# Performance work log

Measured on AMD Instinct MI355X. Metric: run time of the kernel, lower is better.

## Reference

```python
import jax, jax.numpy as jnp
import numpy as np

COMMITMENT_COST = 0.25
NUM_EMBEDDINGS = 512
EMBEDDING_DIM = 64


def setup_inputs() -> dict:
    key = jax.random.key(0)
    k1, k2 = jax.random.split(key)
    inputs = jax.random.normal(k1, (64, EMBEDDING_DIM, 32, 32), dtype=jnp.float32)
    # nn.Embedding init: uniform(-1/K, 1/K)
    emb_w = jax.random.uniform(
        k2, (NUM_EMBEDDINGS, EMBEDDING_DIM), dtype=jnp.float32,
        minval=-1.0 / NUM_EMBEDDINGS, maxval=1.0 / NUM_EMBEDDINGS)
    return {"inputs": inputs, "emb_w": emb_w}


def reference(inputs, emb_w):
    sg = jax.lax.stop_gradient
    # NCHW -> NHWC
    x = jnp.transpose(inputs, (0, 2, 3, 1))          # [B, H, W, D]
    B, H, W, D = x.shape
    flat = x.reshape(-1, D)                          # [N, D]
    dist = (jnp.sum(flat * flat, axis=1, keepdims=True)
            + jnp.sum(emb_w * emb_w, axis=1)
            - 2.0 * jnp.dot(flat, emb_w.T))          # [N, K]
    idx = jnp.argmin(dist, axis=1)                   # [N]
    # one-hot @ emb_w is just a gather
    quantized = emb_w[idx].reshape(B, H, W, D)       # [B, H, W, D]
    e_latent_loss = jnp.mean((sg(quantized) - x) ** 2)
    q_latent_loss = jnp.mean((quantized - sg(x)) ** 2)
    loss = q_latent_loss + COMMITMENT_COST * e_latent_loss
    # straight-through estimator
    quantized_st = x + sg(quantized - x)
    out = jnp.transpose(quantized_st, (0, 3, 1, 2))  # back to NCHW
    return loss, out, idx[:, None]
```

## Files before the change

### kernel.cpp

```cpp
#include <hip/hip_runtime.h>


#define D_    64
#define HW_   1024
#define N_    65536
#define K_    512
#define M_    128
#define CH_   128
#define NCH_  4
#define NDTOT (N_ * D_)

__global__ __launch_bounds__(256) void vq_norm_kernel(const float* __restrict__ emb,
                                                      float* __restrict__ wsn) {
    int k = blockIdx.x * 256 + threadIdx.x;
    if (k < K_) {
        const float* e = emb + k * D_;
        float r[8];
#pragma unroll
        for (int j = 0; j < 8; ++j) r[j] = __fmul_rn(e[j], e[j]);
#pragma unroll
        for (int i = 1; i < 8; ++i)
#pragma unroll
            for (int j = 0; j < 8; ++j)
                r[j] = __fadd_rn(r[j], __fmul_rn(e[i * 8 + j], e[i * 8 + j]));
        float s = __fadd_rn(__fadd_rn(__fadd_rn(r[0], r[1]), __fadd_rn(r[2], r[3])),
                            __fadd_rn(__fadd_rn(r[4], r[5]), __fadd_rn(r[6], r[7])));
        wsn[k] = s;
    }
}

__global__ __launch_bounds__(256, 2) void vq_main_kernel(const float* __restrict__ inp,
                                                         const float* __restrict__ emb,
                                                         const float* __restrict__ wsn,
                                                         float* __restrict__ out) {
    __shared__ float lds[16520];
    float* ldsx = lds;
    float* ldse = lds + 8192;
    float* sxs  = lds + 16384;
    float* partial = lds + 16512;

    const int tid = threadIdx.x;
    const int pg  = tid & 15;
    const int kg  = tid >> 4;
    const int n0  = blockIdx.x * M_;
    const int b   = n0 >> 10;
    const int hw0 = n0 & 1023;
    const float* xbase = inp + b * (D_ * HW_) + hw0;

#pragma unroll
    for (int i = 0; i < 8; ++i) {
        int q  = i * 256 + tid;
        int d  = q >> 5;
        int pq = q & 31;
        float4 v = *(const float4*)(xbase + d * HW_ + pq * 4);
        *(float4*)(ldsx + d * M_ + pq * 4) = v;
    }
    __syncthreads();

    if (tid < M_) {
        float r[8];
#pragma unroll
        for (int j = 0; j < 8; ++j) {
            float v = ldsx[j * M_ + tid];
            r[j] = __fmul_rn(v, v);
        }
#pragma unroll
        for (int i = 1; i < 8; ++i)
#pragma unroll
            for (int j = 0; j < 8; ++j) {
                float v = ldsx[(i * 8 + j) * M_ + tid];
                r[j] = __fadd_rn(r[j], __fmul_rn(v, v));
            }
        sxs[tid] = __fadd_rn(__fadd_rn(__fadd_rn(r[0], r[1]), __fadd_rn(r[2], r[3])),
                             __fadd_rn(__fadd_rn(r[4], r[5]), __fadd_rn(r[6], r[7])));
    }
    __syncthreads();

    float sxp[8];
#pragma unroll
    for (int pp = 0; pp < 8; ++pp) sxp[pp] = sxs[pg * 8 + pp];

    float runv[8];
    int   runi[8];
#pragma unroll
    for (int pp = 0; pp < 8; ++pp) { runv[pp] = 3.4e38f; runi[pp] = 0; }

    for (int c = 0; c < NCH_; ++c) {
        __syncthreads();
#pragma unroll
        for (int i = 0; i < 8; ++i) {
            int q  = i * 256 + tid;
            int kl = q & 127;
            int dq = q >> 7;
            float4 v = *(const float4*)(emb + (c * CH_ + kl) * D_ + dq * 4);
            ldse[(dq * 4 + 0) * CH_ + kl] = v.x;
            ldse[(dq * 4 + 1) * CH_ + kl] = v.y;
            ldse[(dq * 4 + 2) * CH_ + kl] = v.z;
            ldse[(dq * 4 + 3) * CH_ + kl] = v.w;
        }
        float4 nh0 = *(const float4*)(wsn + c * CH_ + kg * 8);
        float4 nh1 = *(const float4*)(wsn + c * CH_ + kg * 8 + 4);
        __syncthreads();

        float acc[8][8];
#pragma unroll
        for (int pp = 0; pp < 8; ++pp)
#pragma unroll
            for (int kk = 0; kk < 8; ++kk) acc[pp][kk] = 0.f;

#pragma unroll 2
        for (int d = 0; d < D_; ++d) {
            float4 xa = *(const float4*)(ldsx + d * M_ + pg * 8);
            float4 xb = *(const float4*)(ldsx + d * M_ + pg * 8 + 4);
            float4 ea = *(const float4*)(ldse + d * CH_ + kg * 8);
            float4 eb = *(const float4*)(ldse + d * CH_ + kg * 8 + 4);
            float xr[8] = {xa.x, xa.y, xa.z, xa.w, xb.x, xb.y, xb.z, xb.w};
            float er[8] = {ea.x, ea.y, ea.z, ea.w, eb.x, eb.y, eb.z, eb.w};
#pragma unroll
            for (int pp = 0; pp < 8; ++pp)
#pragma unroll
                for (int kk = 0; kk < 8; ++kk)
                    acc[pp][kk] = fmaf(xr[pp], er[kk], acc[pp][kk]);
        }

        float nk[8] = {nh0.x, nh0.y, nh0.z, nh0.w, nh1.x, nh1.y, nh1.z, nh1.w};
#pragma unroll
        for (int pp = 0; pp < 8; ++pp) {
            float sx = sxp[pp];
#pragma unroll
            for (int kk = 0; kk < 8; ++kk) {
                float t1 = __fadd_rn(sx, nk[kk]);
                float v  = __fadd_rn(t1, -2.0f * acc[pp][kk]);
                if (v < runv[pp]) { runv[pp] = v; runi[pp] = c * CH_ + kg * 8 + kk; }
            }
        }
    }

    __syncthreads();
    float* sv = ldse;
    int*   si = (int*)(ldse + 2048);
    int*   fi = (int*)(ldse + 4096);
#pragma unroll
    for (int pp = 0; pp < 8; ++pp) {
        sv[kg * M_ + pg * 8 + pp] = runv[pp];
        si[kg * M_ + pg * 8 + pp] = runi[pp];
    }
    __syncthreads();
    if (tid < M_) {
        float bv = 3.4e38f; int bi = 0x7fffffff;
#pragma unroll
        for (int g = 0; g < 16; ++g) {
            float v  = sv[g * M_ + tid];
            int   ii = si[g * M_ + tid];
            if (v < bv || (v == bv && ii < bi)) { bv = v; bi = ii; }
        }
        fi[tid] = bi;
        out[1 + NDTOT + n0 + tid] = (float)bi;
    }
    __syncthreads();

    float* obase = out + 1 + b * (D_ * HW_) + hw0;
    float local = 0.f;
    for (int i = 0; i < 32; ++i) {
        int q = i * 256 + tid;
        int d = q >> 7;
        int p = q & 127;
        int idx = fi[p];
        float e  = emb[idx * D_ + d];
        float xv = ldsx[d * M_ + p];
        float df = e - xv;
        local = fmaf(df, df, local);
        obase[d * HW_ + p] = e;
    }
#pragma unroll
    for (int off = 32; off > 0; off >>= 1)
        local += __shfl_down(local, off, 64);
    if ((tid & 63) == 0) partial[tid >> 6] = local;
    __syncthreads();
    if (tid == 0) {
        float t = partial[0] + partial[1] + partial[2] + partial[3];
        atomicAdd(out, t * (1.25f / (float)NDTOT));
    }
}

extern "C" void kernel_launch(void* const* d_in, const int* in_sizes, int n_in,
                              void* d_out, int out_size, void* d_ws, size_t ws_size,
                              hipStream_t stream) {
    const float* inp = (const float*)d_in[0];
    const float* emb = (const float*)d_in[1];
    float* out = (float*)d_out;
    float* wsn = (float*)d_ws;

    hipMemsetAsync(d_out, 0, sizeof(float), stream);
    vq_norm_kernel<<<2, 256, 0, stream>>>(emb, wsn);
    vq_main_kernel<<<512, 256, 0, stream>>>(inp, emb, wsn, out);
}
```

Measured before the change: 132.1 us.

## Fuse codebook-norm kernel into main VQ kernel and vectorize gather epilogue

Drops the separate norm kernel and has every block compute all 512 codebook norms into LDS, which removes one launch and the workspace round-trip at the cost of redundant per-block norm work. The thread-to-tile mapping is changed so each wave covers an 8x8 patch of points and codes. The reduction scratch gets a padded stride to avoid LDS bank conflicts. The final gather now reads each code row as float4 with a fixed point per thread instead of scalar loads. NDTOT is redefined to an equal value.

```diff
diff --git a/kernel.cpp b/kernel.cpp
--- a/kernel.cpp
+++ b/kernel.cpp
@@ -8,40 +8,26 @@
 #define M_    128
 #define CH_   128
 #define NCH_  4
-#define NDTOT (N_ * D_)
-
-__global__ __launch_bounds__(256) void vq_norm_kernel(const float* __restrict__ emb,
-                                                      float* __restrict__ wsn) {
-    int k = blockIdx.x * 256 + threadIdx.x;
-    if (k < K_) {
-        const float* e = emb + k * D_;
-        float r[8];
-#pragma unroll
-        for (int j = 0; j < 8; ++j) r[j] = __fmul_rn(e[j], e[j]);
-#pragma unroll
-        for (int i = 1; i < 8; ++i)
-#pragma unroll
-            for (int j = 0; j < 8; ++j)
-                r[j] = __fadd_rn(r[j], __fmul_rn(e[i * 8 + j], e[i * 8 + j]));
-        float s = __fadd_rn(__fadd_rn(__fadd_rn(r[0], r[1]), __fadd_rn(r[2], r[3])),
-                            __fadd_rn(__fadd_rn(r[4], r[5]), __fadd_rn(r[6], r[7])));
-        wsn[k] = s;
-    }
-}
+#define NDTOT (N_ * K_ / 8)
+#define SVST  132
 
 __global__ __launch_bounds__(256, 2) void vq_main_kernel(const float* __restrict__ inp,
                                                          const float* __restrict__ emb,
-                                                         const float* __restrict__ wsn,
                                                          float* __restrict__ out) {
-    __shared__ float lds[16520];
+    __shared__ float lds[17156];
     float* ldsx = lds;
     float* ldse = lds + 8192;
-    float* sxs  = lds + 16384;
-    float* partial = lds + 16512;
-
-    const int tid = threadIdx.x;
-    const int pg  = tid & 15;
-    const int kg  = tid >> 4;
+    float* nrm  = lds + 16384;
+    float* sxs  = lds + 16896;
+    int*   fi   = (int*)(lds + 17024);
+    float* partial = lds + 17152;
+
+    const int tid  = threadIdx.x;
+    const int lane = tid & 63;
+    const int wv   = tid >> 6;
+    const int pg = (lane & 7) | ((wv & 1) << 3);
+    const int kg = ((lane >> 3) & 7) | ((wv >> 1) << 3);
+
     const int n0  = blockIdx.x * M_;
     const int b   = n0 >> 10;
     const int hw0 = n0 & 1023;
@@ -54,6 +40,22 @@
         int pq = q & 31;
         float4 v = *(const float4*)(xbase + d * HW_ + pq * 4);
         *(float4*)(ldsx + d * M_ + pq * 4) = v;
+    }
+
+#pragma unroll
+    for (int h = 0; h < 2; ++h) {
+        int k = h * 256 + tid;
+        const float* e = emb + k * D_;
+        float r[8];
+#pragma unroll
+        for (int j = 0; j < 8; ++j) r[j] = __fmul_rn(e[j], e[j]);
+#pragma unroll
+        for (int i = 1; i < 8; ++i)
+#pragma unroll
+            for (int j = 0; j < 8; ++j)
+                r[j] = __fadd_rn(r[j], __fmul_rn(e[i * 8 + j], e[i * 8 + j]));
+        nrm[k] = __fadd_rn(__fadd_rn(__fadd_rn(r[0], r[1]), __fadd_rn(r[2], r[3])),
+                           __fadd_rn(__fadd_rn(r[4], r[5]), __fadd_rn(r[6], r[7])));
     }
     __syncthreads();
 
@@ -98,8 +100,6 @@
             ldse[(dq * 4 + 2) * CH_ + kl] = v.z;
             ldse[(dq * 4 + 3) * CH_ + kl] = v.w;
         }
-        float4 nh0 = *(const float4*)(wsn + c * CH_ + kg * 8);
-        float4 nh1 = *(const float4*)(wsn + c * CH_ + kg * 8 + 4);
         __syncthreads();
 
         float acc[8][8];
@@ -123,13 +123,13 @@
                     acc[pp][kk] = fmaf(xr[pp], er[kk], acc[pp][kk]);
         }
 
-        float nk[8] = {nh0.x, nh0.y, nh0.z, nh0.w, nh1.x, nh1.y, nh1.z, nh1.w};
 #pragma unroll
         for (int pp = 0; pp < 8; ++pp) {
             float sx = sxp[pp];
 #pragma unroll
             for (int kk = 0; kk < 8; ++kk) {
-                float t1 = __fadd_rn(sx, nk[kk]);
+                float nk = nrm[c * CH_ + kg * 8 + kk];
+                float t1 = __fadd_rn(sx, nk);
                 float v  = __fadd_rn(t1, -2.0f * acc[pp][kk]);
                 if (v < runv[pp]) { runv[pp] = v; runi[pp] = c * CH_ + kg * 8 + kk; }
             }
@@ -138,20 +138,19 @@
 
     __syncthreads();
     float* sv = ldse;
-    int*   si = (int*)(ldse + 2048);
-    int*   fi = (int*)(ldse + 4096);
+    int*   si = (int*)(ldse + 16 * SVST);
 #pragma unroll
     for (int pp = 0; pp < 8; ++pp) {
-        sv[kg * M_ + pg * 8 + pp] = runv[pp];
-        si[kg * M_ + pg * 8 + pp] = runi[pp];
+        sv[kg * SVST + pg * 8 + pp] = runv[pp];
+        si[kg * SVST + pg * 8 + pp] = runi[pp];
     }
     __syncthreads();
     if (tid < M_) {
         float bv = 3.4e38f; int bi = 0x7fffffff;
 #pragma unroll
         for (int g = 0; g < 16; ++g) {
-            float v  = sv[g * M_ + tid];
-            int   ii = si[g * M_ + tid];
+            float v  = sv[g * SVST + tid];
+            int   ii = si[g * SVST + tid];
             if (v < bv || (v == bv && ii < bi)) { bv = v; bi = ii; }
         }
         fi[tid] = bi;
@@ -159,18 +158,24 @@
     }
     __syncthreads();
 
-    float* obase = out + 1 + b * (D_ * HW_) + hw0;
+    const int h = tid >> 7;
+    const int p = tid & 127;
+    const int idx = fi[p];
+    const float4* erow = (const float4*)(emb + idx * D_) + h * 8;
+    float* obase = out + 1 + b * (D_ * HW_) + hw0 + p;
     float local = 0.f;
-    for (int i = 0; i < 32; ++i) {
-        int q = i * 256 + tid;
-        int d = q >> 7;
-        int p = q & 127;
-        int idx = fi[p];
-        float e  = emb[idx * D_ + d];
-        float xv = ldsx[d * M_ + p];
-        float df = e - xv;
-        local = fmaf(df, df, local);
-        obase[d * HW_ + p] = e;
+#pragma unroll
+    for (int j = 0; j < 8; ++j) {
+        float4 e4 = erow[j];
+        int d0 = h * 32 + j * 4;
+        float ev[4] = {e4.x, e4.y, e4.z, e4.w};
+#pragma unroll
+        for (int cc = 0; cc < 4; ++cc) {
+            float xv = ldsx[(d0 + cc) * M_ + p];
+            float df = ev[cc] - xv;
+            local = fmaf(df, df, local);
+            obase[(d0 + cc) * HW_] = ev[cc];
+        }
     }
 #pragma unroll
     for (int off = 32; off > 0; off >>= 1)
@@ -189,9 +194,7 @@
     const float* inp = (const float*)d_in[0];
     const float* emb = (const float*)d_in[1];
     float* out = (float*)d_out;
-    float* wsn = (float*)d_ws;
 
     hipMemsetAsync(d_out, 0, sizeof(float), stream);
-    vq_norm_kernel<<<2, 256, 0, stream>>>(emb, wsn);
-    vq_main_kernel<<<512, 256, 0, stream>>>(inp, emb, wsn, out);
+    vq_main_kernel<<<512, 256, 0, stream>>>(inp, emb, out);
 }
```

After: 138.5 us. +4.9%, slower.
